# Kernel optimization log

Measured on AMD Instinct MI355X. Metric: run time of the kernel, lower is better.

The kernel has to match this reference:

```python
import jax, jax.numpy as jnp
import numpy as np

N_ATOM_TYPES = 100
N_BOND_TYPES = 10
N_NODES = 10000
N_EDGES = 320000
N_CAND = 100000
HID = 256
N_MP = 3


def setup_inputs() -> dict:
    key = jax.random.key(0)
    ks = jax.random.split(key, 16)
    d = HID
    inp = {
        "atom_types": jax.random.randint(ks[0], (N_NODES,), 0, N_ATOM_TYPES),
        "bond_types": jax.random.randint(ks[1], (N_EDGES,), 0, N_BOND_TYPES),
        "edge_index": jax.random.randint(ks[2], (2, N_EDGES), 0, N_NODES),
        "candidates": jax.random.randint(ks[3], (N_CAND, 2), 0, N_NODES),
        # parameters (weights stored as [in, out]; bias [out])
        "atom_embed": jax.random.normal(ks[4], (N_ATOM_TYPES, d)) * 0.02,
        "atom_W": jax.random.normal(ks[5], (d, d)) / np.sqrt(d),
        "atom_b": jnp.zeros((d,)),
        "bond_embed": jax.random.normal(ks[6], (N_BOND_TYPES, d)) * 0.02,
        "bond_W": jax.random.normal(ks[7], (d, d)) / np.sqrt(d),
        "bond_b": jnp.zeros((d,)),
        "conv_W": jax.random.normal(ks[8], (N_MP, d, d)) / np.sqrt(d),
        "conv_b": jnp.zeros((N_MP, d)),
        "s_W1": jax.random.normal(ks[9], (2 * d, d)) / np.sqrt(2 * d),
        "s_b1": jnp.zeros((d,)),
        "s_W2": jax.random.normal(ks[10], (d, 1)) / np.sqrt(d),
        "s_b2": jnp.zeros((1,)),
    }
    return inp


def _wln_forward(atom_types, bond_types, edge_index, candidates,
                 atom_embed, atom_W, atom_b, bond_embed, bond_W, bond_b,
                 conv_W, conv_b, s_W1, s_b1, s_W2, s_b2):
    # encoders
    h = atom_embed[atom_types] @ atom_W + atom_b            # [N, d]
    e = bond_embed[bond_types] @ bond_W + bond_b            # [E, d] (unused downstream, as in the original forward)
    del e

    src, dst = edge_index[0], edge_index[1]
    n = h.shape[0]
    ones = jnp.ones((src.shape[0],), dtype=h.dtype)
    deg_out = jax.ops.segment_sum(ones, src, num_segments=n)
    deg_in = jax.ops.segment_sum(ones, dst, num_segments=n)
    norm_src = jnp.where(deg_out > 0, deg_out ** -0.5, 0.0)[:, None]  # [N,1]
    norm_dst = jnp.where(deg_in > 0, deg_in ** -0.5, 0.0)[:, None]

    # message passing: DGL GraphConv norm='both' + ReLU
    for i in range(conv_W.shape[0]):
        m = (h * norm_src)[src]                             # [E, d]
        agg = jax.ops.segment_sum(m, dst, num_segments=n)   # [N, d]
        h = jax.nn.relu((agg * norm_dst) @ conv_W[i] + conv_b[i])

    # batched candidate scorer: gather + concat + 2-layer MLP
    u, v = candidates[:, 0], candidates[:, 1]
    pair = jnp.concatenate([h[u], h[v]], axis=-1)           # [C, 2d]
    hid = jax.nn.relu(pair @ s_W1 + s_b1)                   # [C, d]
    scores = hid @ s_W2 + s_b2                              # [C, 1]
    return scores.squeeze(-1)                               # [C]


def reference(atom_types, bond_types, edge_index, candidates,
              atom_embed, atom_W, atom_b, bond_embed, bond_W, bond_b,
              conv_W, conv_b, s_W1, s_b1, s_W2, s_b2):
    return _wln_forward(atom_types, bond_types, edge_index, candidates,
                        atom_embed, atom_W, atom_b, bond_embed, bond_W, bond_b,
                        conv_W, conv_b, s_W1, s_b1, s_W2, s_b2)
```

## Files before the change

### kernel.cpp

```cpp
#include <hip/hip_runtime.h>

#define N_NODES 10000
#define N_EDGES 320000
#define N_CAND  100000
#define HID     256
#define N_MP    3
#define N_ATYPE 100

typedef short bf16x8 __attribute__((ext_vector_type(8)));
typedef float f32x4  __attribute__((ext_vector_type(4)));

static __device__ __forceinline__ float relu_f(float x) { return x > 0.f ? x : 0.f; }

static __device__ __forceinline__ void split_bf16(float s, unsigned short& hi,
                                                  unsigned short& lo)
{
    unsigned u = __float_as_uint(s);
    hi = (unsigned short)(u >> 16);
    float rem = s - __uint_as_float(u & 0xffff0000u);
    unsigned v = __float_as_uint(rem);
    unsigned r = v + 0x7fffu + ((v >> 16) & 1u);
    lo = (unsigned short)(r >> 16);
}

__global__ __launch_bounds__(256) void k_gemm(
    const float* __restrict__ A, const float* __restrict__ B,
    const float* __restrict__ bias, float* __restrict__ C,
    int M, int doRelu)
{
    __shared__ float As[32][64];
    __shared__ float Bs[32][64];
    int tid = threadIdx.x;
    int tx = tid & 15, ty = tid >> 4;
    int mb = blockIdx.x * 64, nb = blockIdx.y * 64;
    float acc[4][4] = {};
    for (int k0 = 0; k0 < 256; k0 += 32) {
        #pragma unroll
        for (int p = 0; p < 2; ++p) {
            int flat = p * 256 + tid;
            int row = flat >> 3, kc = flat & 7;
            float4 av = make_float4(0.f, 0.f, 0.f, 0.f);
            if (mb + row < M)
                av = *(const float4*)(A + (size_t)(mb + row) * 256 + k0 + kc * 4);
            int sc = row ^ (kc << 2);
            As[kc * 4 + 0][sc] = av.x; As[kc * 4 + 1][sc] = av.y;
            As[kc * 4 + 2][sc] = av.z; As[kc * 4 + 3][sc] = av.w;
        }
        #pragma unroll
        for (int p = 0; p < 2; ++p) {
            int flat = p * 256 + tid;
            int row = flat >> 4, c = flat & 15;
            *(float4*)(&Bs[row][c * 4]) =
                *(const float4*)(B + (size_t)(k0 + row) * 256 + nb + c * 4);
        }
        __syncthreads();
        #pragma unroll 16
        for (int k = 0; k < 32; ++k) {
            float4 a4 = *(const float4*)(&As[k][(ty * 4) ^ ((k >> 2) << 2)]);
            float4 b4 = *(const float4*)(&Bs[k][tx * 4]);
            float a[4] = {a4.x, a4.y, a4.z, a4.w};
            float b[4] = {b4.x, b4.y, b4.z, b4.w};
            #pragma unroll
            for (int i = 0; i < 4; ++i)
                #pragma unroll
                for (int j = 0; j < 4; ++j)
                    acc[i][j] = fmaf(a[i], b[j], acc[i][j]);
        }
        __syncthreads();
    }
    #pragma unroll
    for (int i = 0; i < 4; ++i) {
        int row = mb + ty * 4 + i;
        if (row >= M) continue;
        float r[4];
        #pragma unroll
        for (int j = 0; j < 4; ++j) {
            r[j] = acc[i][j] + (bias ? bias[nb + tx * 4 + j] : 0.f);
            if (doRelu) r[j] = relu_f(r[j]);
        }
        *(float4*)(C + (size_t)row * 256 + nb + tx * 4) =
            make_float4(r[0], r[1], r[2], r[3]);
    }
}

__global__ __launch_bounds__(256) void k_prep_w(
    const float* __restrict__ conv_W, const float* __restrict__ s_W1,
    unsigned short* __restrict__ WTh, unsigned short* __restrict__ WTl)
{
    int bid = blockIdx.x;
    int mat = bid >> 6;
    int id  = (bid & 63) * 256 + threadIdx.x;
    int k   = id >> 6;
    int n4  = id & 63;
    const float* src = (mat < 3) ? conv_W + (size_t)mat * 65536
                                 : s_W1 + (size_t)(mat - 3) * 65536;
    float4 w = *(const float4*)(src + (size_t)k * 256 + n4 * 4);
    float ws[4] = {w.x, w.y, w.z, w.w};
    #pragma unroll
    for (int j = 0; j < 4; ++j) {
        unsigned short hi, lo;
        split_bf16(ws[j], hi, lo);
        size_t idx = (size_t)mat * 65536 + (size_t)(n4 * 4 + j) * 256 + k;
        WTh[idx] = hi;
        WTl[idx] = lo;
    }
}

__global__ __launch_bounds__(256) void k_split(
    const float* __restrict__ h, unsigned short* __restrict__ Ah,
    unsigned short* __restrict__ Al)
{
    int i = blockIdx.x * 256 + threadIdx.x;
    float4 v = ((const float4*)h)[i];
    float vs[4] = {v.x, v.y, v.z, v.w};
    unsigned short hs[4], ls[4];
    #pragma unroll
    for (int j = 0; j < 4; ++j) split_bf16(vs[j], hs[j], ls[j]);
    ushort4 hv = make_ushort4(hs[0], hs[1], hs[2], hs[3]);
    ushort4 lv = make_ushort4(ls[0], ls[1], ls[2], ls[3]);
    ((ushort4*)Ah)[i] = hv;
    ((ushort4*)Al)[i] = lv;
}

static __device__ __forceinline__ void mfma_tile(
    const unsigned short* __restrict__ Ah, const unsigned short* __restrict__ Al,
    const unsigned short* __restrict__ Wh, const unsigned short* __restrict__ Wl,
    const float* __restrict__ bias, const float* __restrict__ scale,
    float* __restrict__ C, int M, int mb, int nb, int doRelu)
{
    int l  = threadIdx.x & 63;
    int li = l & 15;
    int g  = l >> 4;

    int r0 = mb + li;       if (r0 >= M) r0 = M - 1;
    int r1 = mb + 16 + li;  if (r1 >= M) r1 = M - 1;
    int c0 = nb + li;
    int c1 = nb + 16 + li;

    const unsigned short* pA0h = Ah + (size_t)r0 * 256 + g * 8;
    const unsigned short* pA1h = Ah + (size_t)r1 * 256 + g * 8;
    const unsigned short* pA0l = Al + (size_t)r0 * 256 + g * 8;
    const unsigned short* pA1l = Al + (size_t)r1 * 256 + g * 8;
    const unsigned short* pB0h = Wh + (size_t)c0 * 256 + g * 8;
    const unsigned short* pB1h = Wh + (size_t)c1 * 256 + g * 8;
    const unsigned short* pB0l = Wl + (size_t)c0 * 256 + g * 8;
    const unsigned short* pB1l = Wl + (size_t)c1 * 256 + g * 8;

    f32x4 acc00 = {0.f, 0.f, 0.f, 0.f};
    f32x4 acc01 = {0.f, 0.f, 0.f, 0.f};
    f32x4 acc10 = {0.f, 0.f, 0.f, 0.f};
    f32x4 acc11 = {0.f, 0.f, 0.f, 0.f};

    #pragma unroll
    for (int ks = 0; ks < 8; ++ks) {
        int o = ks * 32;
        bf16x8 a0h = *(const bf16x8*)(pA0h + o);
        bf16x8 a1h = *(const bf16x8*)(pA1h + o);
        bf16x8 a0l = *(const bf16x8*)(pA0l + o);
        bf16x8 a1l = *(const bf16x8*)(pA1l + o);
        bf16x8 b0h = *(const bf16x8*)(pB0h + o);
        bf16x8 b1h = *(const bf16x8*)(pB1h + o);
        bf16x8 b0l = *(const bf16x8*)(pB0l + o);
        bf16x8 b1l = *(const bf16x8*)(pB1l + o);

        acc00 = __builtin_amdgcn_mfma_f32_16x16x32_bf16(a0h, b0h, acc00, 0, 0, 0);
        acc01 = __builtin_amdgcn_mfma_f32_16x16x32_bf16(a0h, b1h, acc01, 0, 0, 0);
        acc10 = __builtin_amdgcn_mfma_f32_16x16x32_bf16(a1h, b0h, acc10, 0, 0, 0);
        acc11 = __builtin_amdgcn_mfma_f32_16x16x32_bf16(a1h, b1h, acc11, 0, 0, 0);

        acc00 = __builtin_amdgcn_mfma_f32_16x16x32_bf16(a0h, b0l, acc00, 0, 0, 0);
        acc01 = __builtin_amdgcn_mfma_f32_16x16x32_bf16(a0h, b1l, acc01, 0, 0, 0);
        acc10 = __builtin_amdgcn_mfma_f32_16x16x32_bf16(a1h, b0l, acc10, 0, 0, 0);
        acc11 = __builtin_amdgcn_mfma_f32_16x16x32_bf16(a1h, b1l, acc11, 0, 0, 0);

        acc00 = __builtin_amdgcn_mfma_f32_16x16x32_bf16(a0l, b0h, acc00, 0, 0, 0);
        acc01 = __builtin_amdgcn_mfma_f32_16x16x32_bf16(a0l, b1h, acc01, 0, 0, 0);
        acc10 = __builtin_amdgcn_mfma_f32_16x16x32_bf16(a1l, b0h, acc10, 0, 0, 0);
        acc11 = __builtin_amdgcn_mfma_f32_16x16x32_bf16(a1l, b1h, acc11, 0, 0, 0);
    }

    #pragma unroll
    for (int rt = 0; rt < 2; ++rt) {
        #pragma unroll
        for (int ct = 0; ct < 2; ++ct) {
            f32x4 a = rt ? (ct ? acc11 : acc10) : (ct ? acc01 : acc00);
            int col = nb + ct * 16 + li;
            float bv = bias ? bias[col] : 0.f;
            #pragma unroll
            for (int j = 0; j < 4; ++j) {
                int row = mb + rt * 16 + g * 4 + j;
                if (row >= M) continue;
                float v = a[j] + bv;
                if (doRelu) v = relu_f(v);
                if (scale) v *= scale[row];
                C[(size_t)row * 256 + col] = v;
            }
        }
    }
}

__global__ __launch_bounds__(64) void k_gemm_conv_mfma(
    const unsigned short* __restrict__ Ah, const unsigned short* __restrict__ Al,
    const unsigned short* __restrict__ Wh, const unsigned short* __restrict__ Wl,
    const float* __restrict__ bias, const float* __restrict__ scale,
    float* __restrict__ C, int M)
{
    int bid = blockIdx.x;
    int l = bid & 7;
    int r = bid >> 3;
    int y = r & 7;
    int gx = r >> 3;
    int x = gx * 8 + l;
    if (x * 32 >= M) return;
    mfma_tile(Ah, Al, Wh, Wl, bias, scale, C, M, x * 32, y * 32, 1);
}

__global__ __launch_bounds__(64) void k_gemm_pq_mfma(
    const unsigned short* __restrict__ Ah, const unsigned short* __restrict__ Al,
    const unsigned short* __restrict__ WTh, const unsigned short* __restrict__ WTl,
    float* __restrict__ P, float* __restrict__ Q, int M)
{
    int bid = blockIdx.x;
    int l = bid & 7;
    int r = bid >> 3;
    int y = r & 7;
    int t = r >> 3;
    int half = t & 1;
    int gx = t >> 1;
    int x = gx * 8 + l;
    if (x * 32 >= M) return;
    const unsigned short* wh = WTh + (size_t)(3 + half) * 65536;
    const unsigned short* wl = WTl + (size_t)(3 + half) * 65536;
    mfma_tile(Ah, Al, wh, wl, nullptr, nullptr, half ? Q : P, M, x * 32, y * 32, 0);
}

__global__ void k_hist(const int* __restrict__ ei,
                       int* __restrict__ dout, int* __restrict__ din)
{
    int e = blockIdx.x * blockDim.x + threadIdx.x;
    if (e >= N_EDGES) return;
    atomicAdd(&dout[ei[e]], 1);
    atomicAdd(&din[ei[N_EDGES + e]], 1);
}

__global__ void k_norm(const int* __restrict__ dout, const int* __restrict__ din,
                       float* __restrict__ ns, float* __restrict__ nd)
{
    int i = blockIdx.x * blockDim.x + threadIdx.x;
    if (i >= N_NODES) return;
    int o = dout[i], in = din[i];
    ns[i] = (o  > 0) ? (1.0f / sqrtf((float)o))  : 0.f;
    nd[i] = (in > 0) ? (1.0f / sqrtf((float)in)) : 0.f;
}

__global__ __launch_bounds__(256) void k_h0(const int* __restrict__ types,
                                            const float* __restrict__ E0,
                                            const float* __restrict__ ns,
                                            float* __restrict__ h)
{
    int node = blockIdx.x * 4 + (threadIdx.x >> 6);
    int lane = threadIdx.x & 63;
    if (node >= N_NODES) return;
    int t = types[node];
    float s = ns[node];
    float4 v = ((const float4*)E0)[t * 64 + lane];
    v.x *= s; v.y *= s; v.z *= s; v.w *= s;
    ((float4*)h)[node * 64 + lane] = v;
}

__global__ __launch_bounds__(1024) void k_scan(const int* __restrict__ deg,
                                               int* __restrict__ off, int n)
{
    __shared__ int part[1024];
    int t = threadIdx.x;
    int chunk = (n + 1023) / 1024;
    int base = t * chunk;
    int s = 0;
    for (int i = 0; i < chunk; ++i) {
        int idx = base + i;
        if (idx < n) s += deg[idx];
    }
    part[t] = s;
    __syncthreads();
    for (int d = 1; d < 1024; d <<= 1) {
        int v = (t >= d) ? part[t - d] : 0;
        __syncthreads();
        part[t] += v;
        __syncthreads();
    }
    int run = (t == 0) ? 0 : part[t - 1];
    if (t == 0) off[0] = 0;
    for (int i = 0; i < chunk; ++i) {
        int idx = base + i;
        if (idx < n) { run += deg[idx]; off[idx + 1] = run; }
    }
}

__global__ void k_fill(const int* __restrict__ ei, const int* __restrict__ off,
                       int* __restrict__ cur, int* __restrict__ csr)
{
    int e = blockIdx.x * blockDim.x + threadIdx.x;
    if (e >= N_EDGES) return;
    int d = ei[N_EDGES + e];
    int p = off[d] + atomicAdd(&cur[d], 1);
    csr[p] = ei[e];
}

__global__ __launch_bounds__(256) void k_agg(
    const float* __restrict__ h, const float* __restrict__ nd,
    const int* __restrict__ off, const int* __restrict__ csr,
    unsigned short* __restrict__ Ah, unsigned short* __restrict__ Al)
{
    int bid  = blockIdx.x;
    int slot = bid & 7;
    int c    = slot >> 1;
    int p    = ((bid >> 3) << 1) | (slot & 1);
    int wave = threadIdx.x >> 6;
    int lane = threadIdx.x & 63;
    int wi   = p * 4 + wave;
    int col  = c * 64 + lane;

    for (int node = wi; node < N_NODES; node += 2048) {
        int s0 = off[node], s1 = off[node + 1];
        float a0 = 0.f, a1 = 0.f, a2 = 0.f, a3 = 0.f;
        float a4 = 0.f, a5 = 0.f, a6 = 0.f, a7 = 0.f;
        int e = s0;
        for (; e + 8 <= s1; e += 8) {
            int i0 = csr[e],     i1 = csr[e + 1], i2 = csr[e + 2], i3 = csr[e + 3];
            int i4 = csr[e + 4], i5 = csr[e + 5], i6 = csr[e + 6], i7 = csr[e + 7];
            float v0 = h[(size_t)i0 * 256 + col];
            float v1 = h[(size_t)i1 * 256 + col];
            float v2 = h[(size_t)i2 * 256 + col];
            float v3 = h[(size_t)i3 * 256 + col];
            float v4 = h[(size_t)i4 * 256 + col];
            float v5 = h[(size_t)i5 * 256 + col];
            float v6 = h[(size_t)i6 * 256 + col];
            float v7 = h[(size_t)i7 * 256 + col];
            a0 += v0; a1 += v1; a2 += v2; a3 += v3;
            a4 += v4; a5 += v5; a6 += v6; a7 += v7;
        }
        for (; e < s1; ++e)
            a0 += h[(size_t)csr[e] * 256 + col];
        float s = (((a0 + a1) + (a2 + a3)) + ((a4 + a5) + (a6 + a7))) * nd[node];
        unsigned short hi, lo;
        split_bf16(s, hi, lo);
        Ah[(size_t)node * 256 + col] = hi;
        Al[(size_t)node * 256 + col] = lo;
    }
}

__global__ __launch_bounds__(256) void k_score_part(
    const int* __restrict__ cand, const float* __restrict__ P,
    const float* __restrict__ Q, const float* __restrict__ b1,
    const float* __restrict__ W2, float* __restrict__ part)
{
    int bid = blockIdx.x;
    int c   = bid & 7;
    int grp = bid >> 3;
    int cd  = grp * 256 + threadIdx.x;
    if (cd >= N_CAND) return;

    int u = cand[2 * cd];
    int v = cand[2 * cd + 1];
    const float4* P4 = (const float4*)P;
    const float4* Q4 = (const float4*)Q;
    const float4* B4 = (const float4*)b1;
    const float4* W4 = (const float4*)W2;
    size_t pb = (size_t)u * 64 + c * 8;
    size_t qb = (size_t)v * 64 + c * 8;

    float4 p[8], q[8];
    #pragma unroll
    for (int i = 0; i < 8; ++i) p[i] = P4[pb + i];
    #pragma unroll
    for (int i = 0; i < 8; ++i) q[i] = Q4[qb + i];

    float acc = 0.f;
    #pragma unroll
    for (int i = 0; i < 8; ++i) {
        float4 b = B4[c * 8 + i];
        float4 w = W4[c * 8 + i];
        acc = fmaf(relu_f(p[i].x + q[i].x + b.x), w.x, acc);
        acc = fmaf(relu_f(p[i].y + q[i].y + b.y), w.y, acc);
        acc = fmaf(relu_f(p[i].z + q[i].z + b.z), w.z, acc);
        acc = fmaf(relu_f(p[i].w + q[i].w + b.w), w.w, acc);
    }
    part[(size_t)c * N_CAND + cd] = acc;
}

__global__ void k_sred(const float* __restrict__ part,
                       const float* __restrict__ b2, float* __restrict__ out)
{
    int i = blockIdx.x * 256 + threadIdx.x;
    if (i >= N_CAND) return;
    float s = b2[0];
    #pragma unroll
    for (int c = 0; c < 8; ++c) s += part[(size_t)c * N_CAND + i];
    out[i] = s;
}

extern "C" void kernel_launch(void* const* d_in, const int* in_sizes, int n_in,
                              void* d_out, int out_size, void* d_ws, size_t ws_size,
                              hipStream_t stream)
{
    const int*   atom_types = (const int*)d_in[0];
    const int*   edge_index = (const int*)d_in[2];
    const int*   candidates = (const int*)d_in[3];
    const float* atom_embed = (const float*)d_in[4];
    const float* atom_W     = (const float*)d_in[5];
    const float* atom_b     = (const float*)d_in[6];
    const float* conv_W     = (const float*)d_in[10];
    const float* conv_b     = (const float*)d_in[11];
    const float* s_W1       = (const float*)d_in[12];
    const float* s_b1       = (const float*)d_in[13];
    const float* s_W2       = (const float*)d_in[14];
    const float* s_b2       = (const float*)d_in[15];
    float* out = (float*)d_out;

    char* w = (char*)d_ws;
    size_t o = 0;
    auto alloc = [&](size_t bytes) {
        void* p = w + o;
        o += (bytes + 255) & ~(size_t)255;
        return p;
    };
    float*          h0   = (float*)alloc((size_t)N_NODES * HID * 4);
    float*          h1   = (float*)alloc((size_t)N_NODES * HID * 4);
    float*          P    = (float*)alloc((size_t)N_NODES * HID * 4);
    float*          Q    = (float*)alloc((size_t)N_NODES * HID * 4);
    unsigned short* Ah   = (unsigned short*)alloc((size_t)N_NODES * HID * 2);
    unsigned short* Al   = (unsigned short*)alloc((size_t)N_NODES * HID * 2);
    unsigned short* WTh  = (unsigned short*)alloc((size_t)5 * 65536 * 2);
    unsigned short* WTl  = (unsigned short*)alloc((size_t)5 * 65536 * 2);
    float*          E0   = (float*)alloc((size_t)N_ATYPE * HID * 4);
    float*          part = (float*)alloc((size_t)8 * N_CAND * 4);
    int*            ints = (int*)alloc((size_t)3 * N_NODES * 4);
    float*          ns   = (float*)alloc((size_t)N_NODES * 4);
    float*          nd   = (float*)alloc((size_t)N_NODES * 4);
    int*            off  = (int*)alloc((size_t)(N_NODES + 1) * 4);
    int*            csr  = (int*)alloc((size_t)N_EDGES * 4);
    int* dego = ints;
    int* degi = ints + N_NODES;
    int* cur  = ints + 2 * N_NODES;

    hipMemsetAsync(ints, 0, (size_t)3 * N_NODES * 4, stream);

    k_gemm<<<dim3(2, 4), 256, 0, stream>>>(atom_embed, atom_W, atom_b, E0, N_ATYPE, 0);
    k_prep_w<<<320, 256, 0, stream>>>(conv_W, s_W1, WTh, WTl);

    k_hist<<<(N_EDGES + 255) / 256, 256, 0, stream>>>(edge_index, dego, degi);
    k_norm<<<(N_NODES + 255) / 256, 256, 0, stream>>>(dego, degi, ns, nd);
    k_h0<<<N_NODES / 4, 256, 0, stream>>>(atom_types, E0, ns, h0);
    k_scan<<<1, 1024, 0, stream>>>(degi, off, N_NODES);
    k_fill<<<(N_EDGES + 255) / 256, 256, 0, stream>>>(edge_index, off, cur, csr);

    const float* hc = h0;
    float* hn = h1;
    for (int i = 0; i < N_MP; ++i) {
        k_agg<<<2048, 256, 0, stream>>>(hc, nd, off, csr, Ah, Al);
        const float* sc = (i < N_MP - 1) ? ns : nullptr;
        k_gemm_conv_mfma<<<2560, 64, 0, stream>>>(
            Ah, Al, WTh + (size_t)i * 65536, WTl + (size_t)i * 65536,
            conv_b + (size_t)i * HID, sc, hn, N_NODES);
        float* t = (float*)hc; hc = hn; hn = t;
    }
    k_split<<<2500, 256, 0, stream>>>(hc, Ah, Al);
    k_gemm_pq_mfma<<<5120, 64, 0, stream>>>(Ah, Al, WTh, WTl, P, Q, N_NODES);

    k_score_part<<<3128, 256, 0, stream>>>(candidates, P, Q, s_b1, s_W2, part);
    k_sred<<<(N_CAND + 255) / 256, 256, 0, stream>>>(part, s_b2, out);
}
```

Baseline: 356.8 us.

## Fuse whole WLN pipeline into one persistent kernel with grid barriers

Replaces about fifteen separate launches (histogram, norm, scan, CSR fill, aggregation, MFMA GEMMs, scoring, reduction) with one persistent kernel of 512 blocks. Phases are separated by a software grid barrier built on an atomic counter. The scan becomes a two-level per-block prefix sum, and the last conv GEMM writes bf16 hi/lo splits directly, which removes the separate split pass. This targets launch gaps and tail effects, but adds barrier spin cost, gives the gather-heavy aggregation less parallelism, and assumes all blocks are co-resident.

```diff
diff --git a/kernel.cpp b/kernel.cpp
--- a/kernel.cpp
+++ b/kernel.cpp
@@ -6,6 +6,12 @@
 #define HID     256
 #define N_MP    3
 #define N_ATYPE 100
+
+#define MG_BLOCKS  512
+#define MG_THREADS 256
+#define MG_NT      (MG_BLOCKS * MG_THREADS)
+#define MG_NW      (MG_NT / 64)
+#define NPB        20
 
 typedef short bf16x8 __attribute__((ext_vector_type(8)));
 typedef float f32x4  __attribute__((ext_vector_type(4)));
@@ -23,110 +29,27 @@
     lo = (unsigned short)(r >> 16);
 }
 
-__global__ __launch_bounds__(256) void k_gemm(
-    const float* __restrict__ A, const float* __restrict__ B,
-    const float* __restrict__ bias, float* __restrict__ C,
-    int M, int doRelu)
+static __device__ __forceinline__ void gsync(unsigned* ctr)
 {
-    __shared__ float As[32][64];
-    __shared__ float Bs[32][64];
-    int tid = threadIdx.x;
-    int tx = tid & 15, ty = tid >> 4;
-    int mb = blockIdx.x * 64, nb = blockIdx.y * 64;
-    float acc[4][4] = {};
-    for (int k0 = 0; k0 < 256; k0 += 32) {
-        #pragma unroll
-        for (int p = 0; p < 2; ++p) {
-            int flat = p * 256 + tid;
-            int row = flat >> 3, kc = flat & 7;
-            float4 av = make_float4(0.f, 0.f, 0.f, 0.f);
-            if (mb + row < M)
-                av = *(const float4*)(A + (size_t)(mb + row) * 256 + k0 + kc * 4);
-            int sc = row ^ (kc << 2);
-            As[kc * 4 + 0][sc] = av.x; As[kc * 4 + 1][sc] = av.y;
-            As[kc * 4 + 2][sc] = av.z; As[kc * 4 + 3][sc] = av.w;
-        }
-        #pragma unroll
-        for (int p = 0; p < 2; ++p) {
-            int flat = p * 256 + tid;
-            int row = flat >> 4, c = flat & 15;
-            *(float4*)(&Bs[row][c * 4]) =
-                *(const float4*)(B + (size_t)(k0 + row) * 256 + nb + c * 4);
-        }
-        __syncthreads();
-        #pragma unroll 16
-        for (int k = 0; k < 32; ++k) {
-            float4 a4 = *(const float4*)(&As[k][(ty * 4) ^ ((k >> 2) << 2)]);
-            float4 b4 = *(const float4*)(&Bs[k][tx * 4]);
-            float a[4] = {a4.x, a4.y, a4.z, a4.w};
-            float b[4] = {b4.x, b4.y, b4.z, b4.w};
-            #pragma unroll
-            for (int i = 0; i < 4; ++i)
-                #pragma unroll
-                for (int j = 0; j < 4; ++j)
-                    acc[i][j] = fmaf(a[i], b[j], acc[i][j]);
-        }
-        __syncthreads();
-    }
-    #pragma unroll
-    for (int i = 0; i < 4; ++i) {
-        int row = mb + ty * 4 + i;
-        if (row >= M) continue;
-        float r[4];
-        #pragma unroll
-        for (int j = 0; j < 4; ++j) {
-            r[j] = acc[i][j] + (bias ? bias[nb + tx * 4 + j] : 0.f);
-            if (doRelu) r[j] = relu_f(r[j]);
-        }
-        *(float4*)(C + (size_t)row * 256 + nb + tx * 4) =
-            make_float4(r[0], r[1], r[2], r[3]);
-    }
-}
-
-__global__ __launch_bounds__(256) void k_prep_w(
-    const float* __restrict__ conv_W, const float* __restrict__ s_W1,
-    unsigned short* __restrict__ WTh, unsigned short* __restrict__ WTl)
-{
-    int bid = blockIdx.x;
-    int mat = bid >> 6;
-    int id  = (bid & 63) * 256 + threadIdx.x;
-    int k   = id >> 6;
-    int n4  = id & 63;
-    const float* src = (mat < 3) ? conv_W + (size_t)mat * 65536
-                                 : s_W1 + (size_t)(mat - 3) * 65536;
-    float4 w = *(const float4*)(src + (size_t)k * 256 + n4 * 4);
-    float ws[4] = {w.x, w.y, w.z, w.w};
-    #pragma unroll
-    for (int j = 0; j < 4; ++j) {
-        unsigned short hi, lo;
-        split_bf16(ws[j], hi, lo);
-        size_t idx = (size_t)mat * 65536 + (size_t)(n4 * 4 + j) * 256 + k;
-        WTh[idx] = hi;
-        WTl[idx] = lo;
-    }
-}
-
-__global__ __launch_bounds__(256) void k_split(
-    const float* __restrict__ h, unsigned short* __restrict__ Ah,
-    unsigned short* __restrict__ Al)
-{
-    int i = blockIdx.x * 256 + threadIdx.x;
-    float4 v = ((const float4*)h)[i];
-    float vs[4] = {v.x, v.y, v.z, v.w};
-    unsigned short hs[4], ls[4];
-    #pragma unroll
-    for (int j = 0; j < 4; ++j) split_bf16(vs[j], hs[j], ls[j]);
-    ushort4 hv = make_ushort4(hs[0], hs[1], hs[2], hs[3]);
-    ushort4 lv = make_ushort4(ls[0], ls[1], ls[2], ls[3]);
-    ((ushort4*)Ah)[i] = hv;
-    ((ushort4*)Al)[i] = lv;
+    __syncthreads();
+    if (threadIdx.x == 0) {
+        __threadfence();
+        unsigned ticket = atomicAdd(ctr, 1u);
+        unsigned target = (ticket / MG_BLOCKS + 1u) * MG_BLOCKS;
+        while (atomicAdd(ctr, 0u) < target)
+            __builtin_amdgcn_s_sleep(2);
+        __threadfence();
+    }
+    __syncthreads();
 }
 
 static __device__ __forceinline__ void mfma_tile(
     const unsigned short* __restrict__ Ah, const unsigned short* __restrict__ Al,
     const unsigned short* __restrict__ Wh, const unsigned short* __restrict__ Wl,
     const float* __restrict__ bias, const float* __restrict__ scale,
-    float* __restrict__ C, int M, int mb, int nb, int doRelu)
+    float* __restrict__ outF, unsigned short* __restrict__ outH,
+    unsigned short* __restrict__ outL,
+    int M, int mb, int nb, int doRelu)
 {
     int l  = threadIdx.x & 63;
     int li = l & 15;
@@ -193,210 +116,243 @@
                 float v = a[j] + bv;
                 if (doRelu) v = relu_f(v);
                 if (scale) v *= scale[row];
-                C[(size_t)row * 256 + col] = v;
+                if (outF) {
+                    outF[(size_t)row * 256 + col] = v;
+                } else {
+                    unsigned short hi, lo;
+                    split_bf16(v, hi, lo);
+                    outH[(size_t)row * 256 + col] = hi;
+                    outL[(size_t)row * 256 + col] = lo;
+                }
             }
         }
     }
 }
 
-__global__ __launch_bounds__(64) void k_gemm_conv_mfma(
-    const unsigned short* __restrict__ Ah, const unsigned short* __restrict__ Al,
-    const unsigned short* __restrict__ Wh, const unsigned short* __restrict__ Wl,
-    const float* __restrict__ bias, const float* __restrict__ scale,
-    float* __restrict__ C, int M)
+struct MegaParams {
+    const int*   atom_types;
+    const int*   edge_index;
+    const int*   candidates;
+    const float* atom_embed;
+    const float* atom_W;
+    const float* atom_b;
+    const float* conv_W;
+    const float* conv_b;
+    const float* s_W1;
+    const float* s_b1;
+    const float* s_W2;
+    const float* s_b2;
+    float* E0; float* h0; float* h1; float* Pm; float* Qm;
+    float* ns; float* nd; float* part; float* out;
+    unsigned short* Ah; unsigned short* Al;
+    unsigned short* Ah2; unsigned short* Al2;
+    unsigned short* WTh; unsigned short* WTl;
+    int* dego; int* degi; int* cur; int* off; int* csr;
+    int* bsum; int* bpre;
+    unsigned* bar;
+};
+
+__global__ __launch_bounds__(MG_THREADS, 4) void k_mega(MegaParams P)
 {
-    int bid = blockIdx.x;
-    int l = bid & 7;
-    int r = bid >> 3;
-    int y = r & 7;
-    int gx = r >> 3;
-    int x = gx * 8 + l;
-    if (x * 32 >= M) return;
-    mfma_tile(Ah, Al, Wh, Wl, bias, scale, C, M, x * 32, y * 32, 1);
-}
-
-__global__ __launch_bounds__(64) void k_gemm_pq_mfma(
-    const unsigned short* __restrict__ Ah, const unsigned short* __restrict__ Al,
-    const unsigned short* __restrict__ WTh, const unsigned short* __restrict__ WTl,
-    float* __restrict__ P, float* __restrict__ Q, int M)
-{
-    int bid = blockIdx.x;
-    int l = bid & 7;
-    int r = bid >> 3;
-    int y = r & 7;
-    int t = r >> 3;
-    int half = t & 1;
-    int gx = t >> 1;
-    int x = gx * 8 + l;
-    if (x * 32 >= M) return;
-    const unsigned short* wh = WTh + (size_t)(3 + half) * 65536;
-    const unsigned short* wl = WTl + (size_t)(3 + half) * 65536;
-    mfma_tile(Ah, Al, wh, wl, nullptr, nullptr, half ? Q : P, M, x * 32, y * 32, 0);
-}
-
-__global__ void k_hist(const int* __restrict__ ei,
-                       int* __restrict__ dout, int* __restrict__ din)
-{
-    int e = blockIdx.x * blockDim.x + threadIdx.x;
-    if (e >= N_EDGES) return;
-    atomicAdd(&dout[ei[e]], 1);
-    atomicAdd(&din[ei[N_EDGES + e]], 1);
-}
-
-__global__ void k_norm(const int* __restrict__ dout, const int* __restrict__ din,
-                       float* __restrict__ ns, float* __restrict__ nd)
-{
-    int i = blockIdx.x * blockDim.x + threadIdx.x;
-    if (i >= N_NODES) return;
-    int o = dout[i], in = din[i];
-    ns[i] = (o  > 0) ? (1.0f / sqrtf((float)o))  : 0.f;
-    nd[i] = (in > 0) ? (1.0f / sqrtf((float)in)) : 0.f;
-}
-
-__global__ __launch_bounds__(256) void k_h0(const int* __restrict__ types,
-                                            const float* __restrict__ E0,
-                                            const float* __restrict__ ns,
-                                            float* __restrict__ h)
-{
-    int node = blockIdx.x * 4 + (threadIdx.x >> 6);
-    int lane = threadIdx.x & 63;
-    if (node >= N_NODES) return;
-    int t = types[node];
-    float s = ns[node];
-    float4 v = ((const float4*)E0)[t * 64 + lane];
-    v.x *= s; v.y *= s; v.z *= s; v.w *= s;
-    ((float4*)h)[node * 64 + lane] = v;
-}
-
-__global__ __launch_bounds__(1024) void k_scan(const int* __restrict__ deg,
-                                               int* __restrict__ off, int n)
-{
-    __shared__ int part[1024];
-    int t = threadIdx.x;
-    int chunk = (n + 1023) / 1024;
-    int base = t * chunk;
-    int s = 0;
-    for (int i = 0; i < chunk; ++i) {
-        int idx = base + i;
-        if (idx < n) s += deg[idx];
-    }
-    part[t] = s;
-    __syncthreads();
-    for (int d = 1; d < 1024; d <<= 1) {
-        int v = (t >= d) ? part[t - d] : 0;
+    const int tid  = blockIdx.x * MG_THREADS + threadIdx.x;
+    const int wid  = tid >> 6;
+    const int lane = threadIdx.x & 63;
+    __shared__ int sh[256];
+    unsigned* B = P.bar;
+
+    for (int i = tid; i < 3 * N_NODES; i += MG_NT) P.dego[i] = 0;
+    for (int idx = tid; idx < 5 * 65536; idx += MG_NT) {
+        int mat = idx >> 16;
+        int e   = idx & 65535;
+        int n   = e >> 8;
+        int k   = e & 255;
+        const float* src = (mat < 3) ? P.conv_W + (size_t)mat * 65536
+                                     : P.s_W1 + (size_t)(mat - 3) * 65536;
+        unsigned short hi, lo;
+        split_bf16(src[(size_t)k * 256 + n], hi, lo);
+        size_t oi = (size_t)mat * 65536 + (size_t)n * 256 + k;
+        P.WTh[oi] = hi;
+        P.WTl[oi] = lo;
+    }
+    for (int o = tid; o < N_ATYPE * 256; o += MG_NT) {
+        int r = o >> 8, c = o & 255;
+        float acc = P.atom_b[c];
+        for (int k = 0; k < 256; ++k)
+            acc = fmaf(P.atom_embed[(size_t)r * 256 + k],
+                       P.atom_W[(size_t)k * 256 + c], acc);
+        P.E0[(size_t)r * 256 + c] = acc;
+    }
+    gsync(B + 0);
+
+    for (int e = tid; e < N_EDGES; e += MG_NT) {
+        atomicAdd(&P.dego[P.edge_index[e]], 1);
+        atomicAdd(&P.degi[P.edge_index[N_EDGES + e]], 1);
+    }
+    gsync(B + 1);
+
+    for (int node = wid; node < N_NODES; node += MG_NW) {
+        int o  = P.dego[node];
+        int in = P.degi[node];
+        float nsv = (o  > 0) ? (1.0f / sqrtf((float)o))  : 0.f;
+        float ndv = (in > 0) ? (1.0f / sqrtf((float)in)) : 0.f;
+        if (lane == 0) { P.ns[node] = nsv; P.nd[node] = ndv; }
+        int t = P.atom_types[node];
+        float4 v = ((const float4*)P.E0)[(size_t)t * 64 + lane];
+        v.x *= nsv; v.y *= nsv; v.z *= nsv; v.w *= nsv;
+        ((float4*)P.h0)[(size_t)node * 64 + lane] = v;
+    }
+    if (threadIdx.x == 0) {
+        int b = blockIdx.x, s = 0;
+        for (int i = 0; i < NPB; ++i) {
+            int j = b * NPB + i;
+            if (j < N_NODES) s += P.degi[j];
+        }
+        P.bsum[b] = s;
+    }
+    gsync(B + 2);
+
+    if (blockIdx.x == 0) {
+        int t = threadIdx.x;
+        int v0 = P.bsum[2 * t], v1 = P.bsum[2 * t + 1];
+        sh[t] = v0 + v1;
         __syncthreads();
-        part[t] += v;
-        __syncthreads();
-    }
-    int run = (t == 0) ? 0 : part[t - 1];
-    if (t == 0) off[0] = 0;
-    for (int i = 0; i < chunk; ++i) {
-        int idx = base + i;
-        if (idx < n) { run += deg[idx]; off[idx + 1] = run; }
-    }
-}
-
-__global__ void k_fill(const int* __restrict__ ei, const int* __restrict__ off,
-                       int* __restrict__ cur, int* __restrict__ csr)
-{
-    int e = blockIdx.x * blockDim.x + threadIdx.x;
-    if (e >= N_EDGES) return;
-    int d = ei[N_EDGES + e];
-    int p = off[d] + atomicAdd(&cur[d], 1);
-    csr[p] = ei[e];
-}
-
-__global__ __launch_bounds__(256) void k_agg(
-    const float* __restrict__ h, const float* __restrict__ nd,
-    const int* __restrict__ off, const int* __restrict__ csr,
-    unsigned short* __restrict__ Ah, unsigned short* __restrict__ Al)
-{
-    int bid  = blockIdx.x;
-    int slot = bid & 7;
-    int c    = slot >> 1;
-    int p    = ((bid >> 3) << 1) | (slot & 1);
-    int wave = threadIdx.x >> 6;
-    int lane = threadIdx.x & 63;
-    int wi   = p * 4 + wave;
-    int col  = c * 64 + lane;
-
-    for (int node = wi; node < N_NODES; node += 2048) {
-        int s0 = off[node], s1 = off[node + 1];
-        float a0 = 0.f, a1 = 0.f, a2 = 0.f, a3 = 0.f;
-        float a4 = 0.f, a5 = 0.f, a6 = 0.f, a7 = 0.f;
-        int e = s0;
-        for (; e + 8 <= s1; e += 8) {
-            int i0 = csr[e],     i1 = csr[e + 1], i2 = csr[e + 2], i3 = csr[e + 3];
-            int i4 = csr[e + 4], i5 = csr[e + 5], i6 = csr[e + 6], i7 = csr[e + 7];
-            float v0 = h[(size_t)i0 * 256 + col];
-            float v1 = h[(size_t)i1 * 256 + col];
-            float v2 = h[(size_t)i2 * 256 + col];
-            float v3 = h[(size_t)i3 * 256 + col];
-            float v4 = h[(size_t)i4 * 256 + col];
-            float v5 = h[(size_t)i5 * 256 + col];
-            float v6 = h[(size_t)i6 * 256 + col];
-            float v7 = h[(size_t)i7 * 256 + col];
-            a0 += v0; a1 += v1; a2 += v2; a3 += v3;
-            a4 += v4; a5 += v5; a6 += v6; a7 += v7;
-        }
-        for (; e < s1; ++e)
-            a0 += h[(size_t)csr[e] * 256 + col];
-        float s = (((a0 + a1) + (a2 + a3)) + ((a4 + a5) + (a6 + a7))) * nd[node];
-        unsigned short hi, lo;
-        split_bf16(s, hi, lo);
-        Ah[(size_t)node * 256 + col] = hi;
-        Al[(size_t)node * 256 + col] = lo;
-    }
-}
-
-__global__ __launch_bounds__(256) void k_score_part(
-    const int* __restrict__ cand, const float* __restrict__ P,
-    const float* __restrict__ Q, const float* __restrict__ b1,
-    const float* __restrict__ W2, float* __restrict__ part)
-{
-    int bid = blockIdx.x;
-    int c   = bid & 7;
-    int grp = bid >> 3;
-    int cd  = grp * 256 + threadIdx.x;
-    if (cd >= N_CAND) return;
-
-    int u = cand[2 * cd];
-    int v = cand[2 * cd + 1];
-    const float4* P4 = (const float4*)P;
-    const float4* Q4 = (const float4*)Q;
-    const float4* B4 = (const float4*)b1;
-    const float4* W4 = (const float4*)W2;
-    size_t pb = (size_t)u * 64 + c * 8;
-    size_t qb = (size_t)v * 64 + c * 8;
-
-    float4 p[8], q[8];
-    #pragma unroll
-    for (int i = 0; i < 8; ++i) p[i] = P4[pb + i];
-    #pragma unroll
-    for (int i = 0; i < 8; ++i) q[i] = Q4[qb + i];
-
-    float acc = 0.f;
-    #pragma unroll
-    for (int i = 0; i < 8; ++i) {
-        float4 b = B4[c * 8 + i];
-        float4 w = W4[c * 8 + i];
-        acc = fmaf(relu_f(p[i].x + q[i].x + b.x), w.x, acc);
-        acc = fmaf(relu_f(p[i].y + q[i].y + b.y), w.y, acc);
-        acc = fmaf(relu_f(p[i].z + q[i].z + b.z), w.z, acc);
-        acc = fmaf(relu_f(p[i].w + q[i].w + b.w), w.w, acc);
-    }
-    part[(size_t)c * N_CAND + cd] = acc;
-}
-
-__global__ void k_sred(const float* __restrict__ part,
-                       const float* __restrict__ b2, float* __restrict__ out)
-{
-    int i = blockIdx.x * 256 + threadIdx.x;
-    if (i >= N_CAND) return;
-    float s = b2[0];
-    #pragma unroll
-    for (int c = 0; c < 8; ++c) s += part[(size_t)c * N_CAND + i];
-    out[i] = s;
+        for (int d = 1; d < 256; d <<= 1) {
+            int v = (t >= d) ? sh[t - d] : 0;
+            __syncthreads();
+            sh[t] += v;
+            __syncthreads();
+        }
+        int base = (t > 0) ? sh[t - 1] : 0;
+        P.bpre[2 * t]     = base;
+        P.bpre[2 * t + 1] = base + v0;
+    }
+    gsync(B + 3);
+
+    if (threadIdx.x == 0) {
+        int b = blockIdx.x;
+        int run = P.bpre[b];
+        for (int i = 0; i < NPB; ++i) {
+            int j = b * NPB + i;
+            if (j < N_NODES) { P.off[j] = run; run += P.degi[j]; }
+        }
+        if (b == MG_BLOCKS - 1) P.off[N_NODES] = run;
+    }
+    gsync(B + 4);
+
+    for (int e = tid; e < N_EDGES; e += MG_NT) {
+        int d = P.edge_index[N_EDGES + e];
+        int p = P.off[d] + atomicAdd(&P.cur[d], 1);
+        P.csr[p] = P.edge_index[e];
+    }
+    gsync(B + 5);
+
+    const float* hc = P.h0;
+    float* hn = P.h1;
+    int bi = 6;
+    for (int L = 0; L < N_MP; ++L) {
+        {
+            int slot = blockIdx.x & 7;
+            int c    = slot >> 1;
+            int p2   = ((blockIdx.x >> 3) << 1) | (slot & 1);
+            int wv   = threadIdx.x >> 6;
+            int wi   = p2 * 4 + wv;
+            int col  = c * 64 + lane;
+            for (int node = wi; node < N_NODES; node += 512) {
+                int s0 = P.off[node], s1 = P.off[node + 1];
+                float a0 = 0.f, a1 = 0.f, a2 = 0.f, a3 = 0.f;
+                float a4 = 0.f, a5 = 0.f, a6 = 0.f, a7 = 0.f;
+                int e = s0;
+                for (; e + 8 <= s1; e += 8) {
+                    int i0 = P.csr[e],     i1 = P.csr[e + 1];
+                    int i2 = P.csr[e + 2], i3 = P.csr[e + 3];
+                    int i4 = P.csr[e + 4], i5 = P.csr[e + 5];
+                    int i6 = P.csr[e + 6], i7 = P.csr[e + 7];
+                    float v0 = hc[(size_t)i0 * 256 + col];
+                    float v1 = hc[(size_t)i1 * 256 + col];
+                    float v2 = hc[(size_t)i2 * 256 + col];
+                    float v3 = hc[(size_t)i3 * 256 + col];
+                    float v4 = hc[(size_t)i4 * 256 + col];
+                    float v5 = hc[(size_t)i5 * 256 + col];
+                    float v6 = hc[(size_t)i6 * 256 + col];
+                    float v7 = hc[(size_t)i7 * 256 + col];
+                    a0 += v0; a1 += v1; a2 += v2; a3 += v3;
+                    a4 += v4; a5 += v5; a6 += v6; a7 += v7;
+                }
+                for (; e < s1; ++e)
+                    a0 += hc[(size_t)P.csr[e] * 256 + col];
+                float s = (((a0 + a1) + (a2 + a3)) + ((a4 + a5) + (a6 + a7)))
+                          * P.nd[node];
+                unsigned short hi, lo;
+                split_bf16(s, hi, lo);
+                P.Ah[(size_t)node * 256 + col] = hi;
+                P.Al[(size_t)node * 256 + col] = lo;
+            }
+        }
+        gsync(B + bi); ++bi;
+        {
+            const unsigned short* Wh = P.WTh + (size_t)L * 65536;
+            const unsigned short* Wl = P.WTl + (size_t)L * 65536;
+            const float* bias = P.conv_b + (size_t)L * 256;
+            const float* sc   = (L < N_MP - 1) ? P.ns : nullptr;
+            float* outF = (L < N_MP - 1) ? hn : nullptr;
+            for (int t = wid; t < 313 * 8; t += MG_NW) {
+                int x = t >> 3, y = t & 7;
+                mfma_tile(P.Ah, P.Al, Wh, Wl, bias, sc,
+                          outF, P.Ah2, P.Al2, N_NODES, x * 32, y * 32, 1);
+            }
+        }
+        gsync(B + bi); ++bi;
+        const float* tswap = hc; hc = hn; hn = (float*)tswap;
+    }
+
+    for (int t = wid; t < 313 * 16; t += MG_NW) {
+        int x = t >> 4, r = t & 15;
+        int half = r >> 3, y = r & 7;
+        const unsigned short* wh = P.WTh + (size_t)(3 + half) * 65536;
+        const unsigned short* wl = P.WTl + (size_t)(3 + half) * 65536;
+        mfma_tile(P.Ah2, P.Al2, wh, wl, nullptr, nullptr,
+                  half ? P.Qm : P.Pm, nullptr, nullptr, N_NODES, x * 32, y * 32, 0);
+    }
+    gsync(B + 12);
+
+    {
+        int c  = blockIdx.x & 7;
+        int bc = blockIdx.x >> 3;
+        const float4* P4 = (const float4*)P.Pm;
+        const float4* Q4 = (const float4*)P.Qm;
+        const float4* B4 = (const float4*)P.s_b1;
+        const float4* W4 = (const float4*)P.s_W2;
+        for (int cd = bc * 256 + threadIdx.x; cd < N_CAND; cd += 64 * 256) {
+            int u = P.candidates[2 * cd];
+            int v = P.candidates[2 * cd + 1];
+            size_t pb = (size_t)u * 64 + c * 8;
+            size_t qb = (size_t)v * 64 + c * 8;
+            float4 p[8], q[8];
+            #pragma unroll
+            for (int i = 0; i < 8; ++i) p[i] = P4[pb + i];
+            #pragma unroll
+            for (int i = 0; i < 8; ++i) q[i] = Q4[qb + i];
+            float acc = 0.f;
+            #pragma unroll
+            for (int i = 0; i < 8; ++i) {
+                float4 b = B4[c * 8 + i];
+                float4 w = W4[c * 8 + i];
+                acc = fmaf(relu_f(p[i].x + q[i].x + b.x), w.x, acc);
+                acc = fmaf(relu_f(p[i].y + q[i].y + b.y), w.y, acc);
+                acc = fmaf(relu_f(p[i].z + q[i].z + b.z), w.z, acc);
+                acc = fmaf(relu_f(p[i].w + q[i].w + b.w), w.w, acc);
+            }
+            P.part[(size_t)c * N_CAND + cd] = acc;
+        }
+    }
+    gsync(B + 13);
+
+    for (int i = tid; i < N_CAND; i += MG_NT) {
+        float s = P.s_b2[0];
+        #pragma unroll
+        for (int c = 0; c < 8; ++c) s += P.part[(size_t)c * N_CAND + i];
+        P.out[i] = s;
+    }
 }
 
 extern "C" void kernel_launch(void* const* d_in, const int* in_sizes, int n_in,
@@ -426,10 +382,12 @@
     };
     float*          h0   = (float*)alloc((size_t)N_NODES * HID * 4);
     float*          h1   = (float*)alloc((size_t)N_NODES * HID * 4);
-    float*          P    = (float*)alloc((size_t)N_NODES * HID * 4);
-    float*          Q    = (float*)alloc((size_t)N_NODES * HID * 4);
+    float*          Pm   = (float*)alloc((size_t)N_NODES * HID * 4);
+    float*          Qm   = (float*)alloc((size_t)N_NODES * HID * 4);
     unsigned short* Ah   = (unsigned short*)alloc((size_t)N_NODES * HID * 2);
     unsigned short* Al   = (unsigned short*)alloc((size_t)N_NODES * HID * 2);
+    unsigned short* Ah2  = (unsigned short*)alloc((size_t)N_NODES * HID * 2);
+    unsigned short* Al2  = (unsigned short*)alloc((size_t)N_NODES * HID * 2);
     unsigned short* WTh  = (unsigned short*)alloc((size_t)5 * 65536 * 2);
     unsigned short* WTl  = (unsigned short*)alloc((size_t)5 * 65536 * 2);
     float*          E0   = (float*)alloc((size_t)N_ATYPE * HID * 4);
@@ -439,34 +397,25 @@
     float*          nd   = (float*)alloc((size_t)N_NODES * 4);
     int*            off  = (int*)alloc((size_t)(N_NODES + 1) * 4);
     int*            csr  = (int*)alloc((size_t)N_EDGES * 4);
-    int* dego = ints;
-    int* degi = ints + N_NODES;
-    int* cur  = ints + 2 * N_NODES;
-
-    hipMemsetAsync(ints, 0, (size_t)3 * N_NODES * 4, stream);
-
-    k_gemm<<<dim3(2, 4), 256, 0, stream>>>(atom_embed, atom_W, atom_b, E0, N_ATYPE, 0);
-    k_prep_w<<<320, 256, 0, stream>>>(conv_W, s_W1, WTh, WTl);
-
-    k_hist<<<(N_EDGES + 255) / 256, 256, 0, stream>>>(edge_index, dego, degi);
-    k_norm<<<(N_NODES + 255) / 256, 256, 0, stream>>>(dego, degi, ns, nd);
-    k_h0<<<N_NODES / 4, 256, 0, stream>>>(atom_types, E0, ns, h0);
-    k_scan<<<1, 1024, 0, stream>>>(degi, off, N_NODES);
-    k_fill<<<(N_EDGES + 255) / 256, 256, 0, stream>>>(edge_index, off, cur, csr);
-
-    const float* hc = h0;
-    float* hn = h1;
-    for (int i = 0; i < N_MP; ++i) {
-        k_agg<<<2048, 256, 0, stream>>>(hc, nd, off, csr, Ah, Al);
-        const float* sc = (i < N_MP - 1) ? ns : nullptr;
-        k_gemm_conv_mfma<<<2560, 64, 0, stream>>>(
-            Ah, Al, WTh + (size_t)i * 65536, WTl + (size_t)i * 65536,
-            conv_b + (size_t)i * HID, sc, hn, N_NODES);
-        float* t = (float*)hc; hc = hn; hn = t;
-    }
-    k_split<<<2500, 256, 0, stream>>>(hc, Ah, Al);
-    k_gemm_pq_mfma<<<5120, 64, 0, stream>>>(Ah, Al, WTh, WTl, P, Q, N_NODES);
-
-    k_score_part<<<3128, 256, 0, stream>>>(candidates, P, Q, s_b1, s_W2, part);
-    k_sred<<<(N_CAND + 255) / 256, 256, 0, stream>>>(part, s_b2, out);
+    int*            bsum = (int*)alloc((size_t)MG_BLOCKS * 4);
+    int*            bpre = (int*)alloc((size_t)MG_BLOCKS * 4);
+    unsigned*       bar  = (unsigned*)alloc((size_t)32 * 4);
+
+    hipMemsetAsync(bar, 0, 32 * 4, stream);
+
+    MegaParams mp;
+    mp.atom_types = atom_types; mp.edge_index = edge_index;
+    mp.candidates = candidates; mp.atom_embed = atom_embed;
+    mp.atom_W = atom_W; mp.atom_b = atom_b;
+    mp.conv_W = conv_W; mp.conv_b = conv_b;
+    mp.s_W1 = s_W1; mp.s_b1 = s_b1; mp.s_W2 = s_W2; mp.s_b2 = s_b2;
+    mp.E0 = E0; mp.h0 = h0; mp.h1 = h1; mp.Pm = Pm; mp.Qm = Qm;
+    mp.ns = ns; mp.nd = nd; mp.part = part; mp.out = out;
+    mp.Ah = Ah; mp.Al = Al; mp.Ah2 = Ah2; mp.Al2 = Al2;
+    mp.WTh = WTh; mp.WTl = WTl;
+    mp.dego = ints; mp.degi = ints + N_NODES; mp.cur = ints + 2 * N_NODES;
+    mp.off = off; mp.csr = csr; mp.bsum = bsum; mp.bpre = bpre;
+    mp.bar = bar;
+
+    k_mega<<<MG_BLOCKS, MG_THREADS, 0, stream>>>(mp);
 }
```

After: 1.146 ms. +221.3%, slower.
